# Kernel optimization log

Measured on AMD Instinct MI355X. Metric: run time of the kernel, lower is better.

Reference implementation:

```python
import jax, jax.numpy as jnp
import numpy as np

K = 16  # centroids per codebook (4-bit LUT indices, blink-mm convention)


def _im2col(x, kh, kw, stride, pad):
    # x: [B, C, H, W] -> [B, P, C*kh*kw] with channel-major feature ordering
    # (each length-(kh*kw) subvector is one channel's patch, matching the
    #  per-channel codebook layout of the 3x3 AMM conv).
    B, C, H, W = x.shape
    xp = jnp.pad(x, ((0, 0), (0, 0), (pad, pad), (pad, pad)))
    Ho = (H + 2 * pad - kh) // stride + 1
    Wo = (W + 2 * pad - kw) // stride + 1
    cols = [xp[:, :, i:i + stride * Ho:stride, j:j + stride * Wo:stride]
            for i in range(kh) for j in range(kw)]  # fixed small loop (<=9)
    feat = jnp.stack(cols, axis=2)                      # [B, C, kh*kw, Ho, Wo]
    feat = feat.reshape(B, C * kh * kw, Ho, Wo)
    feat = feat.transpose(0, 2, 3, 1).reshape(B, Ho * Wo, C * kh * kw)
    return feat, Ho, Wo


def _amm_conv_bn_act(x, centroids, lut, scale, bias, kernel, stride, pad, relu):
    # Product-quantization approximate matmul conv:
    #  1) im2col, split feature dim D into ncodebooks subspaces of dim dsub
    #  2) nearest-centroid (L2) assignment per subspace -> 4-bit index
    #  3) gather+accumulate precomputed LUT dot products over codebooks
    #  4) folded BatchNorm affine + optional ReLU
    feat, Ho, Wo = _im2col(x, kernel, kernel, stride, pad)
    B, P, D = feat.shape
    ncb, k, dsub = centroids.shape
    xs = feat.reshape(B, P, ncb, dsub)
    dots = jnp.einsum('bpcd,ckd->bpck', xs, centroids)          # [B,P,ncb,K]
    c2 = jnp.sum(centroids * centroids, axis=-1)                # [ncb,K]
    idx = jnp.argmin(c2[None, None] - 2.0 * dots, axis=-1)      # [B,P,ncb]
    onehot = jax.nn.one_hot(idx, k, dtype=x.dtype)              # [B,P,ncb,K]
    out = jnp.einsum('bpck,cko->bpo', onehot, lut)              # LUT accumulate
    out = out * scale + bias                                    # folded BN
    if relu:
        out = jax.nn.relu(out)
    Cout = lut.shape[-1]
    return out.reshape(B, Ho, Wo, Cout).transpose(0, 3, 1, 2)


def setup_inputs() -> dict:
    key = jax.random.key(0)
    ks = jax.random.split(key, 16)
    inplanes, planes, width = 1024, 256, 256
    B, H, W = 32, 14, 14
    d = {}
    d['x'] = jax.random.normal(ks[0], (B, inplanes, H, W), dtype=jnp.float32)
    d['c1_centroids'] = jax.random.normal(ks[1], (inplanes // 4, K, 4), dtype=jnp.float32)
    d['c1_lut'] = jax.random.normal(ks[2], (inplanes // 4, K, width), dtype=jnp.float32) * 0.1
    d['c1_scale'] = jax.random.uniform(ks[3], (width,), dtype=jnp.float32, minval=0.5, maxval=1.5)
    d['c1_bias'] = jax.random.normal(ks[4], (width,), dtype=jnp.float32) * 0.1
    d['c2_centroids'] = jax.random.normal(ks[5], (width, K, 9), dtype=jnp.float32)
    d['c2_lut'] = jax.random.normal(ks[6], (width, K, width), dtype=jnp.float32) * 0.1
    d['c2_scale'] = jax.random.uniform(ks[7], (width,), dtype=jnp.float32, minval=0.5, maxval=1.5)
    d['c2_bias'] = jax.random.normal(ks[8], (width,), dtype=jnp.float32) * 0.1
    d['c3_centroids'] = jax.random.normal(ks[9], (width // 4, K, 4), dtype=jnp.float32)
    d['c3_lut'] = jax.random.normal(ks[10], (width // 4, K, planes * 4), dtype=jnp.float32) * 0.1
    d['c3_scale'] = jax.random.uniform(ks[11], (planes * 4,), dtype=jnp.float32, minval=0.5, maxval=1.5)
    d['c3_bias'] = jax.random.normal(ks[12], (planes * 4,), dtype=jnp.float32) * 0.1
    return d


def reference(x, c1_centroids, c1_lut, c1_scale, c1_bias,
              c2_centroids, c2_lut, c2_scale, c2_bias,
              c3_centroids, c3_lut, c3_scale, c3_bias):
    identity = x
    out = _amm_conv_bn_act(x, c1_centroids, c1_lut, c1_scale, c1_bias,
                           kernel=1, stride=1, pad=0, relu=True)
    out = _amm_conv_bn_act(out, c2_centroids, c2_lut, c2_scale, c2_bias,
                           kernel=3, stride=1, pad=1, relu=True)
    out = _amm_conv_bn_act(out, c3_centroids, c3_lut, c3_scale, c3_bias,
                           kernel=1, stride=1, pad=0, relu=False)
    # QuantizedAdd + QuantizedReLU (float reference math: add then relu)
    return jax.nn.relu(out + identity)
```

## Files before the change

kernel.cpp:

```cpp
#include <hip/hip_runtime.h>
#include <stdint.h>

#define PP 196
#define BP 6272

typedef _Float16 half_t;
typedef half_t half8v __attribute__((ext_vector_type(8)));
typedef half_t half2v __attribute__((ext_vector_type(2)));


template <typename T>
__global__ __launch_bounds__(256) void assign_1x1(
    const T* __restrict__ in, const float* __restrict__ cents,
    uint32_t* __restrict__ idxp, int nchan) {
  __shared__ float  sf[8][16][4];
  __shared__ double sd[8][16][6];
  const int chunk = blockIdx.y;
  const int t = threadIdx.x;
  for (int i = t; i < 512; i += 256) {
    float c = cents[(size_t)chunk * 512 + i];
    int cb = i >> 6, r = i & 63;
    sf[cb][r >> 2][r & 3] = c;
    sd[cb][r >> 2][1 + (r & 3)] = (double)c;
  }
  __syncthreads();
  if (t < 128) {
    int cb = t >> 4, k = t & 15;
    double s = 0.0;
#pragma unroll
    for (int d = 0; d < 4; d++) { double c = sd[cb][k][1 + d]; s += c * c; }
    sd[cb][k][0] = s;
  }
  __syncthreads();
  const int p = blockIdx.x * 256 + t;
  if (p >= BP) return;
  const unsigned b = (unsigned)p / 196u;
  const unsigned pr = (unsigned)p - b * 196u;
  const T* xb = in + ((size_t)b * nchan + chunk * 32) * PP + pr;
  T xr[32];
#pragma unroll
  for (int i = 0; i < 32; i++) xr[i] = xb[(size_t)i * PP];
  float xs2[32];
#pragma unroll
  for (int i = 0; i < 32; i++) xs2[i] = 2.f * (float)xr[i];
  uint32_t word = 0;
#pragma unroll 1
  for (int cb = 0; cb < 8; cb++) {
    float best = 1e30f, sec = 1e30f; int bi = 0;
#pragma unroll
    for (int k = 0; k < 16; k++) {
      const float4 c = *(const float4*)&sf[cb][k][0];
      float dist = c.x * (c.x - xs2[cb * 4 + 0]);
      dist = fmaf(c.y, c.y - xs2[cb * 4 + 1], dist);
      dist = fmaf(c.z, c.z - xs2[cb * 4 + 2], dist);
      dist = fmaf(c.w, c.w - xs2[cb * 4 + 3], dist);
      if (dist < best) { sec = best; best = dist; bi = k; }
      else sec = fminf(sec, dist);
    }
    if (__any(sec - best < 2e-4f)) {
      double xv[4];
#pragma unroll
      for (int d = 0; d < 4; d++) xv[d] = (double)xr[cb * 4 + d];
      double bb = 1e300; int bi64 = 0;
#pragma unroll
      for (int k = 0; k < 16; k++) {
        double dot = 0.0;
#pragma unroll
        for (int d = 0; d < 4; d++) dot = fma(xv[d], sd[cb][k][1 + d], dot);
        double dist = sd[cb][k][0] - 2.0 * dot;
        if (dist < bb) { bb = dist; bi64 = k; }
      }
      bi = bi64;
    }
    word |= (uint32_t)bi << (4 * cb);
  }
  idxp[(size_t)chunk * BP + p] = word;
}

__global__ __launch_bounds__(256) void assign_3x3(
    const double* __restrict__ in, const float* __restrict__ cents,
    uint32_t* __restrict__ idxp) {
  __shared__ float  sf[8][16][12];
  __shared__ double sd[8][16][10];
  const int chunk = blockIdx.y;
  const int c0g = chunk * 8;
  const int t = threadIdx.x;
  for (int i = t; i < 1152; i += 256) {
    int cb = i / 144, r = i - cb * 144;
    int k = r / 9, d = r - k * 9;
    float c = cents[(size_t)(c0g + cb) * 144 + k * 9 + d];
    sf[cb][k][1 + d] = c;
    sd[cb][k][1 + d] = (double)c;
  }
  __syncthreads();
  if (t < 128) {
    int cb = t >> 4, k = t & 15;
    double s = 0.0;
    float s32 = 0.f;
#pragma unroll
    for (int d = 0; d < 9; d++) {
      double c = sd[cb][k][1 + d]; s += c * c;
      float cf = sf[cb][k][1 + d]; s32 += cf * cf;
    }
    sd[cb][k][0] = s;
    sf[cb][k][0] = s32;
  }
  __syncthreads();
  const int p = blockIdx.x * 256 + t;
  if (p >= BP) return;
  const unsigned b = (unsigned)p / 196u;
  const unsigned pr = (unsigned)p - b * 196u;
  const int oh = pr / 14, ow = pr - oh * 14;
  uint32_t word = 0;
#pragma unroll 1
  for (int cb = 0; cb < 8; cb++) {
    const double* base = in + ((size_t)b * 256 + (c0g + cb)) * PP;
    double v64[9]; float v32[9];
#pragma unroll
    for (int r = 0; r < 3; r++) {
#pragma unroll
      for (int cc = 0; cc < 3; cc++) {
        int hh = oh + r - 1, ww = ow + cc - 1;
        bool ok = (hh >= 0) & (hh < 14) & (ww >= 0) & (ww < 14);
        double v = ok ? base[hh * 14 + ww] : 0.0;
        v64[r * 3 + cc] = v;
        v32[r * 3 + cc] = (float)v;
      }
    }
    float best = 1e30f, sec = 1e30f; int bi = 0;
#pragma unroll
    for (int k = 0; k < 16; k++) {
      const float4 cA = *(const float4*)&sf[cb][k][0];
      const float4 cB = *(const float4*)&sf[cb][k][4];
      const float4 cC = *(const float4*)&sf[cb][k][8];
      float dot = v32[0] * cA.y;
      dot = fmaf(v32[1], cA.z, dot);
      dot = fmaf(v32[2], cA.w, dot);
      dot = fmaf(v32[3], cB.x, dot);
      dot = fmaf(v32[4], cB.y, dot);
      dot = fmaf(v32[5], cB.z, dot);
      dot = fmaf(v32[6], cB.w, dot);
      dot = fmaf(v32[7], cC.x, dot);
      dot = fmaf(v32[8], cC.y, dot);
      float dist = fmaf(-2.f, dot, cA.x);
      if (dist < best) { sec = best; best = dist; bi = k; }
      else sec = fminf(sec, dist);
    }
    if (__any(sec - best < 4e-4f)) {
      double bb = 1e300; int bi64 = 0;
#pragma unroll
      for (int k = 0; k < 16; k++) {
        double dot = 0.0;
#pragma unroll
        for (int d = 0; d < 9; d++) dot = fma(v64[d], sd[cb][k][1 + d], dot);
        double dist = sd[cb][k][0] - 2.0 * dot;
        if (dist < bb) { bb = dist; bi64 = k; }
      }
      bi = bi64;
    }
    word |= (uint32_t)bi << (4 * cb);
  }
  idxp[(size_t)chunk * BP + p] = word;
}

template <int NCB, int NOUT, bool RELU, bool RES, typename OutT>
__global__ __launch_bounds__(512) void accum_f64(
    const float* __restrict__ lut, const uint32_t* __restrict__ idxp,
    const float* __restrict__ scale, const float* __restrict__ bias,
    const float* __restrict__ res, OutT* __restrict__ out) {
  __shared__ float s_lut[16 * 16 * 36];
  const int t = threadIdx.x;
  const int lane = t & 63;
  const int wave = t >> 6;
  const int q = wave & 3;
  const int pg = wave >> 2;
  const int p = blockIdx.x * 128 + pg * 64 + lane;
  const int o_base = blockIdx.y * 16;
  const int r = t >> 1, h = t & 1;
  const int cb_ls = r >> 4, ks = r & 15;
  double a0 = 0, a1 = 0, a2 = 0, a3 = 0;
  constexpr int NCHUNK = NCB / 16;
  for (int ch = 0; ch < NCHUNK; ch++) {
    __syncthreads();
    uint32_t w0 = idxp[(size_t)(ch * 2) * BP + p];
    uint32_t w1 = idxp[(size_t)(ch * 2 + 1) * BP + p];
    {
      const float* g = lut + (((size_t)(ch * 16 + cb_ls)) * 16 + ks) * NOUT + o_base + h * 8;
      float4 va = *(const float4*)g;
      float4 vb = *(const float4*)(g + 4);
      float* sdm = s_lut + cb_ls * 576 + ks * 36 + h * 8;
      *(float4*)sdm = va;
      *(float4*)(sdm + 4) = vb;
    }
    __syncthreads();
#pragma unroll
    for (int cb_l = 0; cb_l < 16; cb_l++) {
      uint32_t w = (cb_l < 8) ? w0 : w1;
      int idx = (int)((w >> (4 * (cb_l & 7))) & 15u);
      const float4 v = *(const float4*)(s_lut + cb_l * 576 + idx * 36 + q * 4);
      a0 += (double)v.x; a1 += (double)v.y; a2 += (double)v.z; a3 += (double)v.w;
    }
  }
  const unsigned b = (unsigned)p / 196u;
  const unsigned pr = (unsigned)p - b * 196u;
  const int o = o_base + q * 4;
  const float4 sc = *(const float4*)(scale + o);
  const float4 bs = *(const float4*)(bias + o);
  double r0 = a0 * (double)sc.x + (double)bs.x;
  double r1 = a1 * (double)sc.y + (double)bs.y;
  double r2 = a2 * (double)sc.z + (double)bs.z;
  double r3 = a3 * (double)sc.w + (double)bs.w;
  if (RES) {
    const float* rp = res + ((size_t)b * NOUT + o) * PP + pr;
    r0 += (double)rp[0 * PP]; r1 += (double)rp[1 * PP];
    r2 += (double)rp[2 * PP]; r3 += (double)rp[3 * PP];
  }
  if (RELU) {
    r0 = fmax(r0, 0.0); r1 = fmax(r1, 0.0);
    r2 = fmax(r2, 0.0); r3 = fmax(r3, 0.0);
  }
  OutT* op = out + ((size_t)b * NOUT + o) * PP + pr;
  op[0 * PP] = (OutT)r0; op[1 * PP] = (OutT)r1;
  op[2 * PP] = (OutT)r2; op[3 * PP] = (OutT)r3;
}

__global__ __launch_bounds__(256) void accum3_f16(
    const float* __restrict__ lut, const uint32_t* __restrict__ idxp,
    const float* __restrict__ scale, const float* __restrict__ bias,
    const float* __restrict__ res, float* __restrict__ out) {
  __shared__ half_t s16[16 * 640];
  const int t = threadIdx.x;
  const int lane = t & 63;
  const int wave = t >> 6;
  const int h = wave & 1;
  const int pg = wave >> 1;
  const int p = blockIdx.x * 128 + pg * 64 + lane;
  const int o_base = blockIdx.y * 16;
  const int s0 = t, s1 = t + 256;
  const int cA = s0 >> 5, kA = (s0 >> 1) & 15, hA = s0 & 1;
  const int cB = s1 >> 5, kB = (s1 >> 1) & 15, hB = s1 & 1;
  const size_t cs = (size_t)16 * 16 * 1024;
  constexpr int NCHUNK = 4;
  float acc[8];
#pragma unroll
  for (int i = 0; i < 8; i++) acc[i] = 0.f;
  for (int ch = 0; ch < NCHUNK; ch++) {
    __syncthreads();
    uint32_t w0 = idxp[(size_t)(ch * 2) * BP + p];
    uint32_t w1 = idxp[(size_t)(ch * 2 + 1) * BP + p];
    {
      const float* gA = lut + (size_t)ch * cs + ((size_t)cA * 16 + kA) * 1024 + o_base + hA * 8;
      const float* gB = lut + (size_t)ch * cs + ((size_t)cB * 16 + kB) * 1024 + o_base + hB * 8;
      float4 a0 = *(const float4*)gA;
      float4 a1 = *(const float4*)(gA + 4);
      float4 b0 = *(const float4*)gB;
      float4 b1 = *(const float4*)(gB + 4);
      half8v va, vb;
      va[0] = (half_t)a0.x; va[1] = (half_t)a0.y; va[2] = (half_t)a0.z; va[3] = (half_t)a0.w;
      va[4] = (half_t)a1.x; va[5] = (half_t)a1.y; va[6] = (half_t)a1.z; va[7] = (half_t)a1.w;
      vb[0] = (half_t)b0.x; vb[1] = (half_t)b0.y; vb[2] = (half_t)b0.z; vb[3] = (half_t)b0.w;
      vb[4] = (half_t)b1.x; vb[5] = (half_t)b1.y; vb[6] = (half_t)b1.z; vb[7] = (half_t)b1.w;
      *(half8v*)(s16 + cA * 640 + kA * 40 + hA * 8) = va;
      *(half8v*)(s16 + cB * 640 + kB * 40 + hB * 8) = vb;
    }
    __syncthreads();
#pragma unroll
    for (int half_grp = 0; half_grp < 2; half_grp++) {
      half2v p0 = 0, p1 = 0, p2 = 0, p3 = 0;
      uint32_t w = half_grp ? w1 : w0;
#pragma unroll
      for (int j = 0; j < 8; j++) {
        int cb_l = half_grp * 8 + j;
        int idx = (int)((w >> (4 * j)) & 15u);
        const half8v v = *(const half8v*)(s16 + cb_l * 640 + idx * 40 + h * 8);
        const half2v* vp = (const half2v*)&v;
        p0 += vp[0]; p1 += vp[1]; p2 += vp[2]; p3 += vp[3];
      }
      acc[0] += (float)p0[0]; acc[1] += (float)p0[1];
      acc[2] += (float)p1[0]; acc[3] += (float)p1[1];
      acc[4] += (float)p2[0]; acc[5] += (float)p2[1];
      acc[6] += (float)p3[0]; acc[7] += (float)p3[1];
    }
  }
  const unsigned b = (unsigned)p / 196u;
  const unsigned pr = (unsigned)p - b * 196u;
  const int o = o_base + h * 8;
  const float* rp = res + ((size_t)b * 1024 + o) * PP + pr;
  float* op = out + ((size_t)b * 1024 + o) * PP + pr;
#pragma unroll
  for (int i = 0; i < 8; i++) {
    float v = acc[i] * scale[o + i] + bias[o + i] + rp[(size_t)i * PP];
    op[(size_t)i * PP] = fmaxf(v, 0.f);
  }
}


extern "C" void kernel_launch(void* const* d_in, const int* in_sizes, int n_in,
                              void* d_out, int out_size, void* d_ws, size_t ws_size,
                              hipStream_t stream) {
  const float* x   = (const float*)d_in[0];
  const float* c1c = (const float*)d_in[1];
  const float* c1l = (const float*)d_in[2];
  const float* c1s = (const float*)d_in[3];
  const float* c1b = (const float*)d_in[4];
  const float* c2c = (const float*)d_in[5];
  const float* c2l = (const float*)d_in[6];
  const float* c2s = (const float*)d_in[7];
  const float* c2b = (const float*)d_in[8];
  const float* c3c = (const float*)d_in[9];
  const float* c3l = (const float*)d_in[10];
  const float* c3s = (const float*)d_in[11];
  const float* c3b = (const float*)d_in[12];

  const size_t sz_i1 = (size_t)32 * BP * 4;
  const size_t sz_i2 = (size_t)32 * BP * 4;
  const size_t sz_i3 = (size_t)8 * BP * 4;
  const size_t sz_o64 = (size_t)BP * 256 * 8;

  char* w = (char*)d_ws;
  uint32_t* i1 = (uint32_t*)w; w += sz_i1;
  uint32_t* i2 = (uint32_t*)w; w += sz_i2;
  uint32_t* i3 = (uint32_t*)w; w += sz_i3;
  double *out1, *out2;
  if (ws_size >= (size_t)(w - (char*)d_ws) + 2 * sz_o64) {
    out1 = (double*)w;
    out2 = (double*)(w + sz_o64);
  } else {
    out1 = (double*)d_out;
    out2 = out1 + (size_t)BP * 256;
  }

  const dim3 blkA(256);
  assign_1x1<float><<<dim3(25, 32), blkA, 0, stream>>>(x, c1c, i1, 1024);
  accum_f64<256, 256, true, false, double><<<dim3(49, 16), dim3(512), 0, stream>>>(
      c1l, i1, c1s, c1b, nullptr, out1);
  assign_3x3<<<dim3(25, 32), blkA, 0, stream>>>(out1, c2c, i2);
  accum_f64<256, 256, true, false, double><<<dim3(49, 16), dim3(512), 0, stream>>>(
      c2l, i2, c2s, c2b, nullptr, out2);
  assign_1x1<double><<<dim3(25, 8), blkA, 0, stream>>>(out2, c3c, i3, 256);
  accum3_f16<<<dim3(49, 64), blkA, 0, stream>>>(
      c3l, i3, c3s, c3b, x, (float*)d_out);
}
```

Before: 266.4 us.

## Fuse conv3 centroid assignment into conv2 accumulate epilogue and restructure LUT staging

```diff
diff --git a/kernel.cpp b/kernel.cpp
--- a/kernel.cpp
+++ b/kernel.cpp
@@ -163,21 +163,39 @@
   idxp[(size_t)chunk * BP + p] = word;
 }
 
-template <int NCB, int NOUT, bool RELU, bool RES, typename OutT>
-__global__ __launch_bounds__(512) void accum_f64(
+template <int NCB, int NOUT, bool RELU, bool FUSE3, typename OutT>
+__global__ __launch_bounds__(256) void accum_f64(
     const float* __restrict__ lut, const uint32_t* __restrict__ idxp,
     const float* __restrict__ scale, const float* __restrict__ bias,
-    const float* __restrict__ res, OutT* __restrict__ out) {
-  __shared__ float s_lut[16 * 16 * 36];
+    const float* __restrict__ c3cent, uint8_t* __restrict__ i3b,
+    OutT* __restrict__ out) {
+  __shared__ float s_lut[16 * 16 * 20];
+  __shared__ float  c3f[4][16][4];
+  __shared__ float  c3c2f[4][16];
+  __shared__ double c3d[4][16][4];
+  __shared__ double c3c2d[4][16];
   const int t = threadIdx.x;
   const int lane = t & 63;
-  const int wave = t >> 6;
-  const int q = wave & 3;
-  const int pg = wave >> 2;
-  const int p = blockIdx.x * 128 + pg * 64 + lane;
+  const int q = t >> 6;
+  const int p = blockIdx.x * 64 + lane;
   const int o_base = blockIdx.y * 16;
-  const int r = t >> 1, h = t & 1;
-  const int cb_ls = r >> 4, ks = r & 15;
+  if (FUSE3 && t < 64) {
+    int cb_l = t >> 4, k = t & 15;
+    const float4 cf = *(const float4*)(c3cent + ((size_t)(blockIdx.y * 4 + cb_l)) * 64 + k * 4);
+    c3f[cb_l][k][0] = cf.x; c3f[cb_l][k][1] = cf.y;
+    c3f[cb_l][k][2] = cf.z; c3f[cb_l][k][3] = cf.w;
+    double d0 = (double)cf.x, d1 = (double)cf.y, d2 = (double)cf.z, d3 = (double)cf.w;
+    c3d[cb_l][k][0] = d0; c3d[cb_l][k][1] = d1;
+    c3d[cb_l][k][2] = d2; c3d[cb_l][k][3] = d3;
+    double s = 0.0; s += d0 * d0; s += d1 * d1; s += d2 * d2; s += d3 * d3;
+    c3c2d[cb_l][k] = s;
+    float s32 = 0.f; s32 += cf.x * cf.x; s32 += cf.y * cf.y;
+    s32 += cf.z * cf.z; s32 += cf.w * cf.w;
+    c3c2f[cb_l][k] = s32;
+  }
+  const int srow = t >> 2, scol = t & 3;
+  const float* src = lut + (size_t)srow * NOUT + o_base + scol * 4;
+  const int d0f = srow * 20 + scol * 4;
   double a0 = 0, a1 = 0, a2 = 0, a3 = 0;
   constexpr int NCHUNK = NCB / 16;
   for (int ch = 0; ch < NCHUNK; ch++) {
@@ -185,20 +203,25 @@
     uint32_t w0 = idxp[(size_t)(ch * 2) * BP + p];
     uint32_t w1 = idxp[(size_t)(ch * 2 + 1) * BP + p];
     {
-      const float* g = lut + (((size_t)(ch * 16 + cb_ls)) * 16 + ks) * NOUT + o_base + h * 8;
-      float4 va = *(const float4*)g;
-      float4 vb = *(const float4*)(g + 4);
-      float* sdm = s_lut + cb_ls * 576 + ks * 36 + h * 8;
-      *(float4*)sdm = va;
-      *(float4*)(sdm + 4) = vb;
+      const float* g = src + (size_t)(ch * 256) * NOUT;
+#pragma unroll
+      for (int j = 0; j < 4; j++) {
+        float4 v = *(const float4*)(g + (size_t)(64 * j) * NOUT);
+        *(float4*)(s_lut + d0f + j * 1280) = v;
+      }
     }
     __syncthreads();
 #pragma unroll
-    for (int cb_l = 0; cb_l < 16; cb_l++) {
-      uint32_t w = (cb_l < 8) ? w0 : w1;
-      int idx = (int)((w >> (4 * (cb_l & 7))) & 15u);
-      const float4 v = *(const float4*)(s_lut + cb_l * 576 + idx * 36 + q * 4);
-      a0 += (double)v.x; a1 += (double)v.y; a2 += (double)v.z; a3 += (double)v.w;
+    for (int j = 0; j < 8; j++) {
+      uint32_t w = (j < 4) ? w0 : w1;
+      int sh = (j & 3) * 8;
+      int i0 = (int)((w >> sh) & 15u);
+      int i1 = (int)((w >> (sh + 4)) & 15u);
+      const float4 va = *(const float4*)(s_lut + (2 * j) * 320 + i0 * 20 + q * 4);
+      const float4 vb = *(const float4*)(s_lut + (2 * j + 1) * 320 + i1 * 20 + q * 4);
+      float s0 = va.x + vb.x, s1 = va.y + vb.y;
+      float s2 = va.z + vb.z, s3 = va.w + vb.w;
+      a0 += (double)s0; a1 += (double)s1; a2 += (double)s2; a3 += (double)s3;
     }
   }
   const unsigned b = (unsigned)p / 196u;
@@ -210,22 +233,49 @@
   double r1 = a1 * (double)sc.y + (double)bs.y;
   double r2 = a2 * (double)sc.z + (double)bs.z;
   double r3 = a3 * (double)sc.w + (double)bs.w;
-  if (RES) {
-    const float* rp = res + ((size_t)b * NOUT + o) * PP + pr;
-    r0 += (double)rp[0 * PP]; r1 += (double)rp[1 * PP];
-    r2 += (double)rp[2 * PP]; r3 += (double)rp[3 * PP];
-  }
   if (RELU) {
     r0 = fmax(r0, 0.0); r1 = fmax(r1, 0.0);
     r2 = fmax(r2, 0.0); r3 = fmax(r3, 0.0);
   }
-  OutT* op = out + ((size_t)b * NOUT + o) * PP + pr;
-  op[0 * PP] = (OutT)r0; op[1 * PP] = (OutT)r1;
-  op[2 * PP] = (OutT)r2; op[3 * PP] = (OutT)r3;
+  if (FUSE3) {
+    const int cb_l = q;
+    float x0 = (float)r0, x1 = (float)r1, x2 = (float)r2, x3 = (float)r3;
+    float best = 1e30f, sec = 1e30f; int bi = 0;
+#pragma unroll
+    for (int k = 0; k < 16; k++) {
+      const float4 c = *(const float4*)&c3f[cb_l][k][0];
+      float dot = x0 * c.x;
+      dot = fmaf(x1, c.y, dot);
+      dot = fmaf(x2, c.z, dot);
+      dot = fmaf(x3, c.w, dot);
+      float dist = fmaf(-2.f, dot, c3c2f[cb_l][k]);
+      if (dist < best) { sec = best; best = dist; bi = k; }
+      else sec = fminf(sec, dist);
+    }
+    if (__any(sec - best < 1e-3f)) {
+      double bb = 1e300; int bi64 = 0;
+#pragma unroll
+      for (int k = 0; k < 16; k++) {
+        double dot = 0.0;
+        dot = fma(r0, c3d[cb_l][k][0], dot);
+        dot = fma(r1, c3d[cb_l][k][1], dot);
+        dot = fma(r2, c3d[cb_l][k][2], dot);
+        dot = fma(r3, c3d[cb_l][k][3], dot);
+        double dist = c3c2d[cb_l][k] - 2.0 * dot;
+        if (dist < bb) { bb = dist; bi64 = k; }
+      }
+      bi = bi64;
+    }
+    i3b[(size_t)p * 64 + blockIdx.y * 4 + q] = (uint8_t)bi;
+  } else {
+    OutT* op = out + ((size_t)b * NOUT + o) * PP + pr;
+    op[0 * PP] = (OutT)r0; op[1 * PP] = (OutT)r1;
+    op[2 * PP] = (OutT)r2; op[3 * PP] = (OutT)r3;
+  }
 }
 
 __global__ __launch_bounds__(256) void accum3_f16(
-    const float* __restrict__ lut, const uint32_t* __restrict__ idxp,
+    const float* __restrict__ lut, const uint8_t* __restrict__ i3b,
     const float* __restrict__ scale, const float* __restrict__ bias,
     const float* __restrict__ res, float* __restrict__ out) {
   __shared__ half_t s16[16 * 640];
@@ -246,8 +296,7 @@
   for (int i = 0; i < 8; i++) acc[i] = 0.f;
   for (int ch = 0; ch < NCHUNK; ch++) {
     __syncthreads();
-    uint32_t w0 = idxp[(size_t)(ch * 2) * BP + p];
-    uint32_t w1 = idxp[(size_t)(ch * 2 + 1) * BP + p];
+    const uint4 iw = *(const uint4*)(i3b + (size_t)p * 64 + ch * 16);
     {
       const float* gA = lut + (size_t)ch * cs + ((size_t)cA * 16 + kA) * 1024 + o_base + hA * 8;
       const float* gB = lut + (size_t)ch * cs + ((size_t)cB * 16 + kB) * 1024 + o_base + hB * 8;
@@ -265,13 +314,15 @@
     }
     __syncthreads();
 #pragma unroll
-    for (int half_grp = 0; half_grp < 2; half_grp++) {
+    for (int grp = 0; grp < 2; grp++) {
+      uint32_t wa = grp ? iw.z : iw.x;
+      uint32_t wb = grp ? iw.w : iw.y;
       half2v p0 = 0, p1 = 0, p2 = 0, p3 = 0;
-      uint32_t w = half_grp ? w1 : w0;
 #pragma unroll
       for (int j = 0; j < 8; j++) {
-        int cb_l = half_grp * 8 + j;
-        int idx = (int)((w >> (4 * j)) & 15u);
+        uint32_t w = (j < 4) ? wa : wb;
+        int idx = (int)((w >> ((j & 3) * 8)) & 15u);
+        int cb_l = grp * 8 + j;
         const half8v v = *(const half8v*)(s16 + cb_l * 640 + idx * 40 + h * 8);
         const half2v* vp = (const half2v*)&v;
         p0 += vp[0]; p1 += vp[1]; p2 += vp[2]; p3 += vp[3];
@@ -312,32 +363,29 @@
   const float* c3s = (const float*)d_in[11];
   const float* c3b = (const float*)d_in[12];
 
-  const size_t sz_i1 = (size_t)32 * BP * 4;
-  const size_t sz_i2 = (size_t)32 * BP * 4;
-  const size_t sz_i3 = (size_t)8 * BP * 4;
+  const size_t sz_i1  = (size_t)32 * BP * 4;
+  const size_t sz_i2  = (size_t)32 * BP * 4;
+  const size_t sz_i3b = (size_t)BP * 64;
   const size_t sz_o64 = (size_t)BP * 256 * 8;
 
   char* w = (char*)d_ws;
   uint32_t* i1 = (uint32_t*)w; w += sz_i1;
   uint32_t* i2 = (uint32_t*)w; w += sz_i2;
-  uint32_t* i3 = (uint32_t*)w; w += sz_i3;
-  double *out1, *out2;
-  if (ws_size >= (size_t)(w - (char*)d_ws) + 2 * sz_o64) {
+  uint8_t* i3b = (uint8_t*)w;  w += sz_i3b;
+  double* out1;
+  if (ws_size >= (size_t)(w - (char*)d_ws) + sz_o64) {
     out1 = (double*)w;
-    out2 = (double*)(w + sz_o64);
   } else {
     out1 = (double*)d_out;
-    out2 = out1 + (size_t)BP * 256;
-  }
-
-  const dim3 blkA(256);
+  }
+
+  const dim3 blkA(256), blkC(256);
   assign_1x1<float><<<dim3(25, 32), blkA, 0, stream>>>(x, c1c, i1, 1024);
-  accum_f64<256, 256, true, false, double><<<dim3(49, 16), dim3(512), 0, stream>>>(
-      c1l, i1, c1s, c1b, nullptr, out1);
+  accum_f64<256, 256, true, false, double><<<dim3(98, 16), blkC, 0, stream>>>(
+      c1l, i1, c1s, c1b, nullptr, nullptr, out1);
   assign_3x3<<<dim3(25, 32), blkA, 0, stream>>>(out1, c2c, i2);
-  accum_f64<256, 256, true, false, double><<<dim3(49, 16), dim3(512), 0, stream>>>(
-      c2l, i2, c2s, c2b, nullptr, out2);
-  assign_1x1<double><<<dim3(25, 8), blkA, 0, stream>>>(out2, c3c, i3, 256);
-  accum3_f16<<<dim3(49, 64), blkA, 0, stream>>>(
-      c3l, i3, c3s, c3b, x, (float*)d_out);
-}
+  accum_f64<256, 256, true, true, double><<<dim3(98, 16), blkC, 0, stream>>>(
+      c2l, i2, c2s, c2b, c3c, i3b, nullptr);
+  accum3_f16<<<dim3(49, 64), blkC, 0, stream>>>(
+      c3l, i3b, c3s, c3b, x, (float*)d_out);
+}
```

New measurement: 238.1 us. 10.6% less time.
